# Kernel optimization log

Measured on AMD Instinct MI355X. Metric: run time of the kernel, lower is better.

## Reference

```python
import jax, jax.numpy as jnp
import numpy as np

# ---- config (mirrors the torch forward's scalar args) ----
NCONF, NATOMS = 1024, 64
NOShfS, NOShfR, NOShfTheta, NOShfA = 16, 16, 16, 16
OEtaS, OEtaR, OEtaA, OZeta = 16.0, 8.0, 8.0, 8.0
L_S, U_S = -4.0, 4.0
L_R, U_R = 0.0, 4.0
L_A, U_A = 0.0, 4.0
L_T, U_T = 0.0, float(np.pi)
NAOV = 4          # p-orbital atomic-orbital vectors
NS = 9            # s coefficients
# upper-triangular pair indices (i<j) in the same row-major order as the torch double loop
_IU, _JU = np.triu_indices(NAOV, k=1)   # 6 pairs


def setup_inputs() -> dict:
    key = jax.random.key(0)
    k1, k2, k3 = jax.random.split(key, 3)
    coefficients = jax.random.normal(k1, (NCONF, NATOMS, 21), dtype=jnp.float32)
    normalization_library = jax.random.normal(k2, (7, 21), dtype=jnp.float32)
    species = jax.random.randint(k3, (NCONF, NATOMS), 0, 7, dtype=jnp.int64)
    return {"coefficients": coefficients,
            "normalization_library": normalization_library,
            "species": species}


def _forward(coefficients):
    nconf, natoms, _ = coefficients.shape
    dt = coefficients.dtype
    s_coeffs = coefficients[..., :NS]                               # [c,n,9]
    p_matrix = coefficients[..., NS:NS + 3 * NAOV].reshape(nconf, natoms, NAOV, 3)

    # --- s-coefficient Gaussian expansion ---
    OShfS = jnp.linspace(L_S, U_S, NOShfS, dtype=dt)                # [S]
    s_aev = jnp.exp(-OEtaS * (s_coeffs[..., None] - OShfS) ** 2)    # [c,n,9,S]
    s_aev = s_aev.reshape(nconf, natoms, NS * NOShfS)

    # --- radial expansion of p-vector norms ---
    p_norms = jnp.linalg.norm(p_matrix, axis=-1)                    # [c,n,4]
    OShfR = jnp.linspace(L_R, U_R, NOShfR, dtype=dt)
    radial_aev = jnp.exp(-OEtaR * (p_norms[..., None] - OShfR) ** 2)
    radial_aev = radial_aev.reshape(nconf, natoms, NAOV * NOShfR)

    # --- pairwise angles between the 4 p-vectors (6 pairs) ---
    zero_mask = jnp.all(jnp.abs(p_matrix) < 1e-12, axis=-1)         # [c,n,4]
    p_hat = jnp.where(zero_mask[..., None], 0.0,
                      p_matrix / p_norms[..., None])
    cos_all = jnp.einsum('cnid,cnjd->cnij', p_hat, p_hat)           # [c,n,4,4]
    cos_pairs = jnp.clip(cos_all[..., _IU, _JU], -0.9999, 0.9999)   # [c,n,6]
    angles = jnp.arccos(cos_pairs)
    avdist = (p_norms[..., _IU] + p_norms[..., _JU]) * 0.5          # [c,n,6]

    # --- angular expansion with radial coupling ---
    OShfTheta = jnp.linspace(L_T, U_T, NOShfTheta, dtype=dt)
    f_theta = (2.0 ** (1.0 - OZeta)) * \
        ((1.0 + jnp.cos(angles[..., None] - OShfTheta)) * 0.5) ** OZeta  # [c,n,6,T]
    OShfA = jnp.linspace(L_A, U_A, NOShfA, dtype=dt)
    f_dist = jnp.exp(-OEtaA * (avdist[..., None] - OShfA) ** 2)          # [c,n,6,A]
    # outer product over (theta, avdist) grids -> [c,n,6,T,A]
    angular_aev = (f_theta[..., :, None] * f_dist[..., None, :])
    angular_aev = angular_aev.reshape(nconf, natoms, angles.shape[-1] * NOShfTheta * NOShfA)

    return jnp.concatenate((s_aev, radial_aev, angular_aev), axis=-1)


def reference(coefficients, normalization_library, species):
    # normalization_library and species are unused on this code path
    # (basis='sp', use_simple_orbital_aev=False), matching the torch source.
    return _forward(coefficients)
```

## Files before the change

kernel.cpp:

```cpp
#include <hip/hip_runtime.h>


namespace {

typedef float f4 __attribute__((ext_vector_type(4)));

constexpr int kPerAtom = 9 * 16 + 4 * 16 + 6 * 16 * 16;
constexpr int kQ = kPerAtom / 4;

__device__ __constant__ float kCosT[16] = {
     1.0f,          0.97814760f,  0.91354546f,  0.80901699f,
     0.66913061f,   0.5f,         0.30901699f,  0.10452846f,
    -0.10452846f,  -0.30901699f, -0.5f,        -0.66913061f,
    -0.80901699f,  -0.91354546f, -0.97814760f, -1.0f };
__device__ __constant__ float kSinT[16] = {
     0.0f,          0.20791169f,  0.40673664f,  0.58778525f,
     0.74314483f,   0.86602540f,  0.95105652f,  0.99452190f,
     0.99452190f,   0.95105652f,  0.86602540f,  0.74314483f,
     0.58778525f,   0.40673664f,  0.20791169f,  0.0f };

__global__ __launch_bounds__(448) void aev_kernel(
    const float* __restrict__ coeff, float* __restrict__ out)
{
    const int atom = blockIdx.x;
    const float* __restrict__ c = coeff + (long long)atom * 21;
    f4* __restrict__ outv =
        reinterpret_cast<f4*>(out + (long long)atom * kPerAtom);

    const int q = threadIdx.x;
    if (q >= kQ) return;

    float r[4];

    if (q < 36) {
        const int e  = q << 2;
        const int i  = e >> 4;
        const int k0 = e & 15;
        const float s = c[i];
#pragma unroll
        for (int u = 0; u < 4; ++u) {
            const float shf = -4.0f + (float)(k0 + u) * (8.0f / 15.0f);
            const float d = s - shf;
            r[u] = __expf(-16.0f * d * d);
        }
    } else if (q < 52) {
        const int e  = (q - 36) << 2;
        const int i  = e >> 4;
        const int k0 = e & 15;
        const float px = c[9 + 3 * i], py = c[10 + 3 * i], pz = c[11 + 3 * i];
        const float n = sqrtf(px * px + py * py + pz * pz);
#pragma unroll
        for (int u = 0; u < 4; ++u) {
            const float shf = (float)(k0 + u) * (4.0f / 15.0f);
            const float d = n - shf;
            r[u] = __expf(-8.0f * d * d);
        }
    } else {
        const int e  = (q - 52) << 2;
        const int p  = e >> 8;
        const int tt = (e >> 4) & 15;
        const int a0 = e & 15;
        const int IU[6] = {0, 0, 0, 1, 1, 2};
        const int JU[6] = {1, 2, 3, 2, 3, 3};
        const int i = IU[p], j = JU[p];
        const float ax = c[9 + 3 * i], ay = c[10 + 3 * i], az = c[11 + 3 * i];
        const float bx = c[9 + 3 * j], by = c[10 + 3 * j], bz = c[11 + 3 * j];
        const float na = sqrtf(ax * ax + ay * ay + az * az);
        const float nb = sqrtf(bx * bx + by * by + bz * bz);
        const bool ma = fabsf(ax) < 1e-12f && fabsf(ay) < 1e-12f && fabsf(az) < 1e-12f;
        const bool mb = fabsf(bx) < 1e-12f && fabsf(by) < 1e-12f && fabsf(bz) < 1e-12f;
        float cc = (ma || mb) ? 0.0f : (ax * bx + ay * by + az * bz) / (na * nb);
        cc = fminf(0.9999f, fmaxf(-0.9999f, cc));
        const float sn = sqrtf(1.0f - cc * cc);
        const float av = 0.5f * (na + nb);
        const float ct = cc * kCosT[tt] + sn * kSinT[tt];
        const float t  = 0.5f * (1.0f + ct);
        const float t2 = t * t, t4 = t2 * t2;
        const float ft = 0.0078125f * (t4 * t4);
#pragma unroll
        for (int u = 0; u < 4; ++u) {
            const float shf = (float)(a0 + u) * (4.0f / 15.0f);
            const float d = av - shf;
            r[u] = ft * __expf(-8.0f * d * d);
        }
    }

    const f4 v = {r[0], r[1], r[2], r[3]};
    __builtin_nontemporal_store(v, &outv[q]);
}

}

extern "C" void kernel_launch(void* const* d_in, const int* in_sizes, int n_in,
                              void* d_out, int out_size, void* d_ws, size_t ws_size,
                              hipStream_t stream) {
    const float* coeff = (const float*)d_in[0];
    float* out = (float*)d_out;
    const int nblocks = 1024 * 64;
    aev_kernel<<<dim3(nblocks), dim3(448), 0, stream>>>(coeff, out);
}
```

Measured before the change: 534.5 us.

## Precompute per-pair angular and distance factors in shared memory

```diff
diff --git a/kernel.cpp b/kernel.cpp
--- a/kernel.cpp
+++ b/kernel.cpp
@@ -5,88 +5,91 @@
 
 typedef float f4 __attribute__((ext_vector_type(4)));
 
-constexpr int kPerAtom = 9 * 16 + 4 * 16 + 6 * 16 * 16;
+constexpr int kPerAtom = 1744;
 constexpr int kQ = kPerAtom / 4;
-
-__device__ __constant__ float kCosT[16] = {
-     1.0f,          0.97814760f,  0.91354546f,  0.80901699f,
-     0.66913061f,   0.5f,         0.30901699f,  0.10452846f,
-    -0.10452846f,  -0.30901699f, -0.5f,        -0.66913061f,
-    -0.80901699f,  -0.91354546f, -0.97814760f, -1.0f };
-__device__ __constant__ float kSinT[16] = {
-     0.0f,          0.20791169f,  0.40673664f,  0.58778525f,
-     0.74314483f,   0.86602540f,  0.95105652f,  0.99452190f,
-     0.99452190f,   0.95105652f,  0.86602540f,  0.74314483f,
-     0.58778525f,   0.40673664f,  0.20791169f,  0.0f };
+constexpr float kPi = 3.14159265358979323846f;
 
 __global__ __launch_bounds__(448) void aev_kernel(
     const float* __restrict__ coeff, float* __restrict__ out)
 {
+    __shared__ float sCC[6], sSN[6], sAV[6];
+    __shared__ float sFT[96];
+    __shared__ float sFD[96];
+
     const int atom = blockIdx.x;
     const float* __restrict__ c = coeff + (long long)atom * 21;
-    f4* __restrict__ outv =
-        reinterpret_cast<f4*>(out + (long long)atom * kPerAtom);
+    const int q = threadIdx.x;
 
-    const int q = threadIdx.x;
-    if (q >= kQ) return;
+    if (q < 6) {
+        const int p = q;
+        const int i = (p < 3) ? 0 : ((p < 5) ? 1 : 2);
+        const int j = (p < 3) ? (p + 1) : ((p < 5) ? (p - 1) : 3);
+        const float ax = c[9 + 3 * i], ay = c[10 + 3 * i], az = c[11 + 3 * i];
+        const float bx = c[9 + 3 * j], by = c[10 + 3 * j], bz = c[11 + 3 * j];
+        const float na2 = ax * ax + ay * ay + az * az;
+        const float nb2 = bx * bx + by * by + bz * bz;
+        const float dot = ax * bx + ay * by + az * bz;
+        const float ia = (na2 > 1e-24f) ? __builtin_amdgcn_rsqf(na2) : 0.0f;
+        const float ib = (nb2 > 1e-24f) ? __builtin_amdgcn_rsqf(nb2) : 0.0f;
+        float cc = dot * ia * ib;
+        cc = fminf(0.9999f, fmaxf(-0.9999f, cc));
+        sCC[p] = cc;
+        sSN[p] = __builtin_amdgcn_sqrtf(1.0f - cc * cc);
+        sAV[p] = 0.5f * (na2 * ia + nb2 * ib);
+    }
+    __syncthreads();
+
+    if (q < 96) {
+        const int p = q >> 4, t = q & 15;
+        const float th = (float)t * (kPi / 15.0f);
+        const float ct = __cosf(th), st = __sinf(th);
+        const float x = 0.5f * (1.0f + sCC[p] * ct + sSN[p] * st);
+        const float x2 = x * x, x4 = x2 * x2;
+        sFT[q] = 0.0078125f * (x4 * x4);
+    } else if (q < 192) {
+        const int idx = q - 96;
+        const int p = idx >> 4, a = idx & 15;
+        const float d = sAV[p] - (float)a * (4.0f / 15.0f);
+        sFD[idx] = __expf(-8.0f * d * d);
+    }
+    __syncthreads();
 
     float r[4];
-
     if (q < 36) {
-        const int e  = q << 2;
-        const int i  = e >> 4;
-        const int k0 = e & 15;
+        const int i  = q >> 2;
+        const int k0 = (q & 3) << 2;
         const float s = c[i];
 #pragma unroll
         for (int u = 0; u < 4; ++u) {
-            const float shf = -4.0f + (float)(k0 + u) * (8.0f / 15.0f);
-            const float d = s - shf;
+            const float d = s - (-4.0f + (float)(k0 + u) * (8.0f / 15.0f));
             r[u] = __expf(-16.0f * d * d);
         }
     } else if (q < 52) {
-        const int e  = (q - 36) << 2;
-        const int i  = e >> 4;
-        const int k0 = e & 15;
+        const int i  = (q - 36) >> 2;
+        const int k0 = ((q - 36) & 3) << 2;
         const float px = c[9 + 3 * i], py = c[10 + 3 * i], pz = c[11 + 3 * i];
-        const float n = sqrtf(px * px + py * py + pz * pz);
+        const float n = __builtin_amdgcn_sqrtf(px * px + py * py + pz * pz);
 #pragma unroll
         for (int u = 0; u < 4; ++u) {
-            const float shf = (float)(k0 + u) * (4.0f / 15.0f);
-            const float d = n - shf;
+            const float d = n - (float)(k0 + u) * (4.0f / 15.0f);
             r[u] = __expf(-8.0f * d * d);
         }
-    } else {
+    } else if (q < kQ) {
         const int e  = (q - 52) << 2;
         const int p  = e >> 8;
         const int tt = (e >> 4) & 15;
         const int a0 = e & 15;
-        const int IU[6] = {0, 0, 0, 1, 1, 2};
-        const int JU[6] = {1, 2, 3, 2, 3, 3};
-        const int i = IU[p], j = JU[p];
-        const float ax = c[9 + 3 * i], ay = c[10 + 3 * i], az = c[11 + 3 * i];
-        const float bx = c[9 + 3 * j], by = c[10 + 3 * j], bz = c[11 + 3 * j];
-        const float na = sqrtf(ax * ax + ay * ay + az * az);
-        const float nb = sqrtf(bx * bx + by * by + bz * bz);
-        const bool ma = fabsf(ax) < 1e-12f && fabsf(ay) < 1e-12f && fabsf(az) < 1e-12f;
-        const bool mb = fabsf(bx) < 1e-12f && fabsf(by) < 1e-12f && fabsf(bz) < 1e-12f;
-        float cc = (ma || mb) ? 0.0f : (ax * bx + ay * by + az * bz) / (na * nb);
-        cc = fminf(0.9999f, fmaxf(-0.9999f, cc));
-        const float sn = sqrtf(1.0f - cc * cc);
-        const float av = 0.5f * (na + nb);
-        const float ct = cc * kCosT[tt] + sn * kSinT[tt];
-        const float t  = 0.5f * (1.0f + ct);
-        const float t2 = t * t, t4 = t2 * t2;
-        const float ft = 0.0078125f * (t4 * t4);
+        const float ft = sFT[p * 16 + tt];
+        const f4 fd = *reinterpret_cast<const f4*>(&sFD[p * 16 + a0]);
 #pragma unroll
-        for (int u = 0; u < 4; ++u) {
-            const float shf = (float)(a0 + u) * (4.0f / 15.0f);
-            const float d = av - shf;
-            r[u] = ft * __expf(-8.0f * d * d);
-        }
+        for (int u = 0; u < 4; ++u) r[u] = ft * fd[u];
     }
 
-    const f4 v = {r[0], r[1], r[2], r[3]};
-    __builtin_nontemporal_store(v, &outv[q]);
+    if (q < kQ) {
+        f4* __restrict__ outv = reinterpret_cast<f4*>(out + (long long)atom * kPerAtom);
+        const f4 v = {r[0], r[1], r[2], r[3]};
+        outv[q] = v;
+    }
 }
 
 }
@@ -96,6 +99,5 @@
                               hipStream_t stream) {
     const float* coeff = (const float*)d_in[0];
     float* out = (float*)d_out;
-    const int nblocks = 1024 * 64;
-    aev_kernel<<<dim3(nblocks), dim3(448), 0, stream>>>(coeff, out);
+    aev_kernel<<<dim3(1024 * 64), dim3(448), 0, stream>>>(coeff, out);
 }
```

Measured after the change: 514.8 us. 3.7% less time.
